# Performance work log

Hardware: AMD Instinct MI355X
Metric: run time of the kernel (lower is better)

## Reference

```python
import jax, jax.numpy as jnp
import numpy as np

B, C, W, H = 1024, 1, 128, 128
NUM_IDS = 64
MARGIN = 0.3


def setup_inputs() -> dict:
    key = jax.random.key(0)
    k1, k2 = jax.random.split(key)
    inputs = jax.random.normal(k1, (B, C, W, H), dtype=jnp.float32)
    targets = jax.random.randint(k2, (B,), 0, NUM_IDS, dtype=jnp.int32)
    return {"inputs": inputs, "targets": targets}


def _dc_align(anchor, other):
    # Batched cross-attention alignment (DCModuleOptimized assumption):
    # modi = softmax(anchor @ other^T / sqrt(h)) @ other, per sample.
    h = anchor.shape[-1]
    scale = 1.0 / jnp.sqrt(jnp.asarray(h, anchor.dtype))
    att = jax.nn.softmax(jnp.einsum('bij,bkj->bik', anchor, other) * scale, axis=-1)
    return jnp.einsum('bik,bkj->bij', att, other)


def reference(inputs, targets):
    b, c, w, h = inputs.shape
    x = inputs.reshape(b, -1)                      # (n, d); requires c == 1 downstream
    n = b
    # Pairwise Euclidean distances, stable clamp as in torch code
    sq = jnp.sum(x * x, axis=1)                    # (n,)
    dist = sq[:, None] + sq[None, :] - 2.0 * (x @ x.T)
    dist = jnp.sqrt(jnp.clip(dist, 1e-12, None))   # (n, n)
    mask = targets[:, None] == targets[None, :]    # (n, n) same-identity mask
    # Vectorized hard mining (replaces the per-row Python loop)
    NEG = jnp.asarray(-1e30, dist.dtype)
    POS = jnp.asarray(1e30, dist.dtype)
    hp_idx = jnp.argmax(jnp.where(mask, dist, NEG), axis=1)   # hardest positive per row
    hn_idx = jnp.argmin(jnp.where(mask, POS, dist), axis=1)   # hardest negative per row
    anchor = x.reshape(b, w, h)
    h_pos = anchor[hp_idx]                         # (b, w, h) gathered hard positives
    h_neg = anchor[hn_idx]                         # (b, w, h) gathered hard negatives
    # DC module applied over the whole batch at once
    modi_pos = _dc_align(anchor, h_pos)
    modi_neg = _dc_align(anchor, h_neg)
    dap = anchor.reshape(b, -1) - modi_pos.reshape(b, -1)
    dan = anchor.reshape(b, -1) - modi_neg.reshape(b, -1)
    dist_ap = jnp.sqrt(jnp.sum(dap * dap, axis=1))
    dist_an = jnp.sqrt(jnp.sum(dan * dan, axis=1))
    # MarginRankingLoss with y = 1: mean(relu(dist_ap - dist_an + margin))
    loss = jnp.mean(jax.nn.relu(dist_ap - dist_an + MARGIN))
    return loss
```

## Files before the change

### kernel.cpp

```cpp
#include <hip/hip_runtime.h>
#include <stdint.h>

#define NSAMP 1024
#define D 16384
#define WH 128
#define MARGIN 0.3f
#define KS 8
#define KSUB (D / KS)
#define SCALE 0.08838834764831845f
#define RSCALE 11.313708498984761f

typedef unsigned int uint;
typedef unsigned short ushort_t;

typedef __attribute__((ext_vector_type(8))) short bf16x8;
typedef __attribute__((ext_vector_type(4))) float f32x4;

__device__ __forceinline__ float bf2f(unsigned short b) {
    return __uint_as_float(((uint)b) << 16);
}
__device__ __forceinline__ unsigned short f2bf(float f) {
    uint u = __float_as_uint(f);
    u += 0x7fffu + ((u >> 16) & 1u);
    return (unsigned short)(u >> 16);
}
__device__ __forceinline__ void gload_lds16(const void* g, void* l) {
    __builtin_amdgcn_global_load_lds(
        (const __attribute__((address_space(1))) uint32_t*)g,
        (__attribute__((address_space(3))) uint32_t*)l, 16, 0, 0);
}
__device__ __forceinline__ bf16x8 bf8_half(bf16x8 v) {
    union { bf16x8 b; uint u[4]; } c;
    c.b = v;
    c.u[0] -= 0x00800080u; c.u[1] -= 0x00800080u;
    c.u[2] -= 0x00800080u; c.u[3] -= 0x00800080u;
    return c.b;
}
__device__ __forceinline__ int lds_off(int row, int col) {
    return row * 256 + ((((col >> 3) ^ (row & 15)) << 4) | ((col & 7) << 1));
}

__global__ __launch_bounds__(256) void k_norms_split(const float* __restrict__ x,
                                                     float* __restrict__ sq,
                                                     ushort_t* __restrict__ xhi,
                                                     ushort_t* __restrict__ xlo) {
    int b = blockIdx.x;
    int tid = threadIdx.x;
    const float* xr = x + (size_t)b * D;
    ushort_t* hr = xhi + (size_t)b * D;
    ushort_t* lr = xlo + (size_t)b * D;
    float s = 0.f;
    #pragma unroll
    for (int m = 0; m < 16; ++m) {
        int e = m * 1024 + tid * 4;
        float4 v = *(const float4*)(xr + e);
        s += v.x * v.x + v.y * v.y + v.z * v.z + v.w * v.w;
        ushort4 h, l;
        h.x = f2bf(v.x); l.x = f2bf(v.x - bf2f(h.x));
        h.y = f2bf(v.y); l.y = f2bf(v.y - bf2f(h.y));
        h.z = f2bf(v.z); l.z = f2bf(v.z - bf2f(h.z));
        h.w = f2bf(v.w); l.w = f2bf(v.w - bf2f(h.w));
        *(ushort4*)(hr + e) = h;
        *(ushort4*)(lr + e) = l;
    }
    for (int off = 32; off; off >>= 1) s += __shfl_down(s, off, 64);
    __shared__ float red[4];
    if ((tid & 63) == 0) red[tid >> 6] = s;
    __syncthreads();
    if (tid == 0) sq[b] = red[0] + red[1] + red[2] + red[3];
}

__global__ __launch_bounds__(256) void k_gram_mfma(const ushort_t* __restrict__ xhi,
                                                   const ushort_t* __restrict__ xlo,
                                                   float* __restrict__ Gp) {
    int lin = blockIdx.x + 8 * blockIdx.y + 64 * blockIdx.z;
    int ks = lin & 7, bi = (lin >> 3) & 7, bj = lin >> 6;
    int i0 = bi * 128, j0 = bj * 128;
    int tid = threadIdx.x;
    int w = tid >> 6, lane = tid & 63;
    int wm = w & 1, wn = w >> 1;
    int quad = lane >> 4, m16 = lane & 15;
    int srow = lane >> 2, sseg = lane & 3;

    __shared__ __align__(16) ushort_t Ahi_s[128 * 32];
    __shared__ __align__(16) ushort_t Bhi_s[128 * 32];
    __shared__ __align__(16) ushort_t Blo_s[128 * 32];

    f32x4 acc[4][4];
    #pragma unroll
    for (int ii = 0; ii < 4; ++ii)
        #pragma unroll
        for (int jj = 0; jj < 4; ++jj)
            acc[ii][jj] = (f32x4){0.f, 0.f, 0.f, 0.f};

    const size_t Abase = (size_t)i0 * D;
    const size_t Bbase = (size_t)j0 * D;

    for (int kb = 0; kb < KSUB / 32; ++kb) {
        int k0 = ks * KSUB + kb * 32;
        #pragma unroll
        for (int c = 0; c < 2; ++c) {
            int r = w * 32 + c * 16 + srow;
            size_t go = (size_t)r * D + k0 + sseg * 8;
            int lo = (w * 32 + c * 16) * 32;
            gload_lds16(xhi + Abase + go, &Ahi_s[lo]);
            gload_lds16(xhi + Bbase + go, &Bhi_s[lo]);
            gload_lds16(xlo + Bbase + go, &Blo_s[lo]);
        }
        __syncthreads();

        bf16x8 ah[4], bh[4], bl[4];
        #pragma unroll
        for (int ii = 0; ii < 4; ++ii) {
            int ar = wm * 64 + ii * 16 + m16;
            ah[ii] = *(const bf16x8*)&Ahi_s[ar * 32 + quad * 8];
        }
        #pragma unroll
        for (int jj = 0; jj < 4; ++jj) {
            int br = wn * 64 + jj * 16 + m16;
            bh[jj] = *(const bf16x8*)&Bhi_s[br * 32 + quad * 8];
            bl[jj] = *(const bf16x8*)&Blo_s[br * 32 + quad * 8];
        }
        #pragma unroll
        for (int ii = 0; ii < 4; ++ii) {
            bf16x8 ahh = bf8_half(ah[ii]);
            #pragma unroll
            for (int jj = 0; jj < 4; ++jj) {
                acc[ii][jj] = __builtin_amdgcn_mfma_f32_16x16x32_bf16(ahh, bh[jj], acc[ii][jj], 0, 0, 0);
                acc[ii][jj] = __builtin_amdgcn_mfma_f32_16x16x32_bf16(ah[ii], bl[jj], acc[ii][jj], 0, 0, 0);
            }
        }
        __syncthreads();
    }

    float* Gb = Gp + (size_t)ks * NSAMP * NSAMP;
    #pragma unroll
    for (int ii = 0; ii < 4; ++ii)
        #pragma unroll
        for (int jj = 0; jj < 4; ++jj) {
            int rg = i0 + wm * 64 + ii * 16 + quad * 4;
            int cg = j0 + wn * 64 + jj * 16 + m16;
            #pragma unroll
            for (int r = 0; r < 4; ++r)
                Gb[(size_t)(rg + r) * NSAMP + cg] = acc[ii][jj][r];
        }
}

__global__ __launch_bounds__(256) void k_fold_sym(const float* __restrict__ Gp,
                                                  float* __restrict__ G) {
    int J = blockIdx.x, I = blockIdx.y;
    int t = threadIdx.x;
    int r = t >> 4, c4 = (t & 15) * 4;
    __shared__ float TJ[64][65];
    float4 sIJ[4];
    #pragma unroll
    for (int rr = 0; rr < 4; ++rr) {
        int row = rr * 16 + r;
        size_t oIJ = (size_t)(I * 64 + row) * NSAMP + J * 64 + c4;
        size_t oJI = (size_t)(J * 64 + row) * NSAMP + I * 64 + c4;
        float4 a = {0.f, 0.f, 0.f, 0.f}, bb = {0.f, 0.f, 0.f, 0.f};
        #pragma unroll
        for (int p = 0; p < KS; ++p) {
            float4 v = *(const float4*)(Gp + (size_t)p * NSAMP * NSAMP + oIJ);
            float4 w = *(const float4*)(Gp + (size_t)p * NSAMP * NSAMP + oJI);
            a.x += v.x; a.y += v.y; a.z += v.z; a.w += v.w;
            bb.x += w.x; bb.y += w.y; bb.z += w.z; bb.w += w.w;
        }
        sIJ[rr] = a;
        TJ[row][c4 + 0] = bb.x; TJ[row][c4 + 1] = bb.y;
        TJ[row][c4 + 2] = bb.z; TJ[row][c4 + 3] = bb.w;
    }
    __syncthreads();
    #pragma unroll
    for (int rr = 0; rr < 4; ++rr) {
        int row = rr * 16 + r;
        float4 v = sIJ[rr];
        v.x += TJ[c4 + 0][row]; v.y += TJ[c4 + 1][row];
        v.z += TJ[c4 + 2][row]; v.w += TJ[c4 + 3][row];
        *(float4*)(G + (size_t)(I * 64 + row) * NSAMP + J * 64 + c4) = v;
    }
}

__global__ void k_select(const float* __restrict__ G,
                         const float* __restrict__ sq, const int* __restrict__ tgt,
                         int* __restrict__ hp, int* __restrict__ hn,
                         float* __restrict__ dsq) {
    int i = blockIdx.x;
    int tid = threadIdx.x;
    float sqi = sq[i];
    int ti = tgt[i];
    float pv = -3.0e38f; int pj = 0x7FFFFFFF;
    float nv = 3.0e38f;  int nj = 0x7FFFFFFF;
    #pragma unroll
    for (int m = 0; m < 4; ++m) {
        int j = tid + 256 * m;
        float g = G[(size_t)i * NSAMP + j];
        float d2 = sqi + sq[j] - 2.f * g;
        float d = sqrtf(fmaxf(d2, 1e-12f));
        bool same = (tgt[j] == ti);
        float cp = same ? d : -1e30f;
        float cn = same ? 1e30f : d;
        if (cp > pv || (cp == pv && j < pj)) { pv = cp; pj = j; }
        if (cn < nv || (cn == nv && j < nj)) { nv = cn; nj = j; }
    }
    for (int off = 32; off; off >>= 1) {
        float opv = __shfl_down(pv, off, 64); int opj = __shfl_down(pj, off, 64);
        float onv = __shfl_down(nv, off, 64); int onj = __shfl_down(nj, off, 64);
        if (opv > pv || (opv == pv && opj < pj)) { pv = opv; pj = opj; }
        if (onv < nv || (onv == nv && onj < nj)) { nv = onv; nj = onj; }
    }
    __shared__ float spv[4], snv[4];
    __shared__ int spj[4], snj[4];
    if ((tid & 63) == 0) { int wv = tid >> 6; spv[wv] = pv; spj[wv] = pj; snv[wv] = nv; snj[wv] = nj; }
    __syncthreads();
    if (tid == 0) {
        for (int wv = 1; wv < 4; ++wv) {
            if (spv[wv] > pv || (spv[wv] == pv && spj[wv] < pj)) { pv = spv[wv]; pj = spj[wv]; }
            if (snv[wv] < nv || (snv[wv] == nv && snj[wv] < nj)) { nv = snv[wv]; nj = snj[wv]; }
        }
        hp[i] = pj; hn[i] = nj;
        dsq[i] = sqi; dsq[NSAMP + i] = sqi;
    }
}

__global__ __launch_bounds__(256) void k_dc_mfma(const ushort_t* __restrict__ xhi,
                                                 const int* __restrict__ hp,
                                                 const int* __restrict__ hn,
                                                 float* __restrict__ dsq) {
    int b = blockIdx.x;
    int which = blockIdx.y;
    int oidx = (which == 0) ? hp[b] : hn[b];
    const ushort_t* Ag = xhi + (size_t)b * D;
    const ushort_t* Og = xhi + (size_t)oidx * D;

    __shared__ __align__(16) char smem[32768];

    int tid = threadIdx.x;
    int wv = tid >> 6, lane = tid & 63;
    int quad = lane >> 4, m16 = lane & 15;

    bf16x8 af[2][4];
    #pragma unroll
    for (int tj2 = 0; tj2 < 2; ++tj2) {
        int r = (2 * wv + tj2) * 16 + m16;
        #pragma unroll
        for (int ks = 0; ks < 4; ++ks)
            af[tj2][ks] = *(const bf16x8*)(Ag + r * WH + ks * 32 + quad * 8);
    }

    uint4 stg[8];
    #pragma unroll
    for (int k = 0; k < 8; ++k)
        stg[k] = *(const uint4*)((const char*)Og + (size_t)(tid + 256 * k) * 16);
    #pragma unroll
    for (int k = 0; k < 8; ++k) {
        int g = tid + 256 * k;
        *(uint4*)(smem + lds_off(g >> 4, (g & 15) * 8)) = stg[k];
    }
    __syncthreads();

    f32x4 accS[8][2];
    #pragma unroll
    for (int ti = 0; ti < 8; ++ti)
        #pragma unroll
        for (int tj2 = 0; tj2 < 2; ++tj2)
            accS[ti][tj2] = (f32x4){0.f, 0.f, 0.f, 0.f};
    #pragma unroll
    for (int ks = 0; ks < 4; ++ks) {
        bf16x8 of[8];
        #pragma unroll
        for (int ti = 0; ti < 8; ++ti)
            of[ti] = *(const bf16x8*)(smem + lds_off(ti * 16 + m16, (ks * 4 + quad) * 8));
        #pragma unroll
        for (int ti = 0; ti < 8; ++ti)
            #pragma unroll
            for (int tj2 = 0; tj2 < 2; ++tj2)
                accS[ti][tj2] = __builtin_amdgcn_mfma_f32_16x16x32_bf16(of[ti], af[tj2][ks], accS[ti][tj2], 0, 0, 0);
    }

    int c0 = (tid & 31) * 4, h0 = (tid >> 5) * 16;
    uint4 trd[4][2];
    #pragma unroll
    for (int j = 0; j < 4; ++j)
        #pragma unroll
        for (int k = 0; k < 2; ++k)
            trd[j][k] = *(const uint4*)(smem + lds_off(c0 + j, h0 + 8 * k));
    __syncthreads();

    #pragma unroll
    for (int i = 0; i < 16; ++i) {
        uint v[4];
        #pragma unroll
        for (int j = 0; j < 4; ++j) {
            uint wo = ((const uint*)&trd[j][i >> 3])[(i >> 1) & 3];
            v[j] = (i & 1) ? (wo >> 16) : (wo & 0xffffu);
        }
        uint2 pk;
        pk.x = v[0] | (v[1] << 16);
        pk.y = v[2] | (v[3] << 16);
        *(uint2*)(smem + lds_off(h0 + i, c0)) = pk;
    }

    float tpart = 0.f;
    bf16x8 pf[2][4];
    #pragma unroll
    for (int tj2 = 0; tj2 < 2; ++tj2) {
        float mx = -3.0e38f;
        #pragma unroll
        for (int ti = 0; ti < 8; ++ti)
            #pragma unroll
            for (int r = 0; r < 4; ++r) {
                float s = accS[ti][tj2][r] * SCALE;
                accS[ti][tj2][r] = s;
                mx = fmaxf(mx, s);
            }
        mx = fmaxf(mx, __shfl_xor(mx, 16, 64));
        mx = fmaxf(mx, __shfl_xor(mx, 32, 64));
        float sum = 0.f, tnum = 0.f;
        #pragma unroll
        for (int ti = 0; ti < 8; ++ti)
            #pragma unroll
            for (int r = 0; r < 4; ++r) {
                float s = accS[ti][tj2][r];
                float e = __expf(s - mx);
                accS[ti][tj2][r] = e;
                sum += e;
                tnum += s * e;
            }
        sum += __shfl_xor(sum, 16, 64);
        sum += __shfl_xor(sum, 32, 64);
        tnum += __shfl_xor(tnum, 16, 64);
        tnum += __shfl_xor(tnum, 32, 64);
        float inv = 1.f / sum;
        tpart += 0.25f * tnum * inv;

        uint Ep[8][2];
        #pragma unroll
        for (int ti = 0; ti < 8; ++ti) {
            Ep[ti][0] = (uint)f2bf(accS[ti][tj2][0] * inv) |
                        ((uint)f2bf(accS[ti][tj2][1] * inv) << 16);
            Ep[ti][1] = (uint)f2bf(accS[ti][tj2][2] * inv) |
                        ((uint)f2bf(accS[ti][tj2][3] * inv) << 16);
        }
        int tih = quad >> 1;
        #pragma unroll
        for (int ks = 0; ks < 4; ++ks) {
            union { uint u[4]; bf16x8 v; } fr;
            #pragma unroll
            for (int k = 0; k < 4; ++k) {
                int src = (((quad << 1) + (k >> 1)) & 3) * 16 + m16;
                int a = __shfl((int)Ep[2 * ks + 0][k & 1], src, 64);
                int bsh = __shfl((int)Ep[2 * ks + 1][k & 1], src, 64);
                fr.u[k] = (uint)((tih == 0) ? a : bsh);
            }
            pf[tj2][ks] = fr.v;
        }
    }
    __syncthreads();

    f32x4 accM[2][8];
    #pragma unroll
    for (int tj2 = 0; tj2 < 2; ++tj2)
        #pragma unroll
        for (int tj = 0; tj < 8; ++tj)
            accM[tj2][tj] = (f32x4){0.f, 0.f, 0.f, 0.f};
    #pragma unroll
    for (int ks = 0; ks < 4; ++ks) {
        bf16x8 otf[8];
        #pragma unroll
        for (int tj = 0; tj < 8; ++tj)
            otf[tj] = *(const bf16x8*)(smem + lds_off(tj * 16 + m16, (ks * 4 + quad) * 8));
        #pragma unroll
        for (int tj2 = 0; tj2 < 2; ++tj2)
            #pragma unroll
            for (int tj = 0; tj < 8; ++tj)
                accM[tj2][tj] = __builtin_amdgcn_mfma_f32_16x16x32_bf16(pf[tj2][ks], otf[tj], accM[tj2][tj], 0, 0, 0);
    }

    float m2 = 0.f;
    #pragma unroll
    for (int tj2 = 0; tj2 < 2; ++tj2)
        #pragma unroll
        for (int tj = 0; tj < 8; ++tj)
            #pragma unroll
            for (int r = 0; r < 4; ++r) {
                float mvv = accM[tj2][tj][r];
                m2 += mvv * mvv;
            }
    float part = m2 - 2.f * RSCALE * tpart;
    for (int off = 32; off; off >>= 1) part += __shfl_down(part, off, 64);
    if (lane == 0) atomicAdd(&dsq[which * NSAMP + b], part);
}

__global__ void k_loss(const float* __restrict__ dsq, float* __restrict__ out) {
    int tid = threadIdx.x;
    float s = 0.f;
    #pragma unroll
    for (int m = 0; m < 4; ++m) {
        int b = tid + 256 * m;
        float ap = sqrtf(fmaxf(dsq[b], 0.f));
        float an = sqrtf(fmaxf(dsq[NSAMP + b], 0.f));
        s += fmaxf(ap - an + MARGIN, 0.f);
    }
    for (int off = 32; off; off >>= 1) s += __shfl_down(s, off, 64);
    __shared__ float red[4];
    if ((tid & 63) == 0) red[tid >> 6] = s;
    __syncthreads();
    if (tid == 0) out[0] = (red[0] + red[1] + red[2] + red[3]) * (1.f / NSAMP);
}

extern "C" void kernel_launch(void* const* d_in, const int* in_sizes, int n_in,
                              void* d_out, int out_size, void* d_ws, size_t ws_size,
                              hipStream_t stream) {
    const float* x = (const float*)d_in[0];
    const int* tgt = (const int*)d_in[1];
    float* out = (float*)d_out;
    char* ws = (char*)d_ws;

    float* Gp = (float*)ws;
    ushort_t* xhi = (ushort_t*)(ws + (size_t)32 * 1024 * 1024);
    ushort_t* xlo = xhi + (size_t)NSAMP * D;
    float* G = (float*)xlo;
    float* sq = (float*)(ws + (size_t)96 * 1024 * 1024);
    float* dsq = sq + NSAMP;
    int* hp = (int*)(dsq + 2 * NSAMP);
    int* hn = hp + NSAMP;

    k_norms_split<<<NSAMP, 256, 0, stream>>>(x, sq, xhi, xlo);
    k_gram_mfma<<<dim3(8, 8, 8), 256, 0, stream>>>(xhi, xlo, Gp);
    k_fold_sym<<<dim3(16, 16), 256, 0, stream>>>(Gp, G);
    k_select<<<NSAMP, 256, 0, stream>>>(G, sq, tgt, hp, hn, dsq);
    k_dc_mfma<<<dim3(NSAMP, 2), 256, 0, stream>>>(xhi, hp, hn, dsq);
    k_loss<<<1, 256, 0, stream>>>(dsq, out);
}
```

Before: 233.3 us.

## Compute only lower-triangular Gram tiles with adaptive split-K and fuse DC passes

The Gram kernel now computes only the 36 lower-triangular 128x128 tiles instead of all 64. Diagonal tiles use a symmetric hi/lo trick, and off-diagonal tiles use three MFMA products. Split-K depth rises to 16 when the workspace allows, and the fold kernel reconstructs the full symmetric matrix from compact per-tile partials. The DC kernel now handles the positive and negative pairs in one block, which replaces the atomics and the dsq initialisation in k_select. The cost is more MFMAs per off-diagonal tile and a second pass through LDS per block.

```diff
diff --git a/kernel.cpp b/kernel.cpp
--- a/kernel.cpp
+++ b/kernel.cpp
@@ -5,8 +5,7 @@
 #define D 16384
 #define WH 128
 #define MARGIN 0.3f
-#define KS 8
-#define KSUB (D / KS)
+#define NTILES 36
 #define SCALE 0.08838834764831845f
 #define RSCALE 11.313708498984761f
 
@@ -70,11 +69,17 @@
     if (tid == 0) sq[b] = red[0] + red[1] + red[2] + red[3];
 }
 
-__global__ __launch_bounds__(256) void k_gram_mfma(const ushort_t* __restrict__ xhi,
-                                                   const ushort_t* __restrict__ xlo,
-                                                   float* __restrict__ Gp) {
-    int lin = blockIdx.x + 8 * blockIdx.y + 64 * blockIdx.z;
-    int ks = lin & 7, bi = (lin >> 3) & 7, bj = lin >> 6;
+__global__ __launch_bounds__(256) void k_gram_tri(const ushort_t* __restrict__ xhi,
+                                                  const ushort_t* __restrict__ xlo,
+                                                  float* __restrict__ Gp,
+                                                  int ksmask, int ksshift, int ksub) {
+    int lin = blockIdx.x;
+    int ks = lin & ksmask;
+    int t = lin >> ksshift;
+    int bi = 0;
+    while (t >= ((bi + 1) * (bi + 2)) / 2) ++bi;
+    int bj = t - (bi * (bi + 1)) / 2;
+    bool diag = (bi == bj);
     int i0 = bi * 128, j0 = bj * 128;
     int tid = threadIdx.x;
     int w = tid >> 6, lane = tid & 63;
@@ -83,6 +88,7 @@
     int srow = lane >> 2, sseg = lane & 3;
 
     __shared__ __align__(16) ushort_t Ahi_s[128 * 32];
+    __shared__ __align__(16) ushort_t Alo_s[128 * 32];
     __shared__ __align__(16) ushort_t Bhi_s[128 * 32];
     __shared__ __align__(16) ushort_t Blo_s[128 * 32];
 
@@ -96,16 +102,19 @@
     const size_t Abase = (size_t)i0 * D;
     const size_t Bbase = (size_t)j0 * D;
 
-    for (int kb = 0; kb < KSUB / 32; ++kb) {
-        int k0 = ks * KSUB + kb * 32;
+    for (int kb = 0; kb < ksub / 32; ++kb) {
+        int k0 = ks * ksub + kb * 32;
         #pragma unroll
         for (int c = 0; c < 2; ++c) {
             int r = w * 32 + c * 16 + srow;
             size_t go = (size_t)r * D + k0 + sseg * 8;
             int lo = (w * 32 + c * 16) * 32;
             gload_lds16(xhi + Abase + go, &Ahi_s[lo]);
-            gload_lds16(xhi + Bbase + go, &Bhi_s[lo]);
             gload_lds16(xlo + Bbase + go, &Blo_s[lo]);
+            if (!diag) {
+                gload_lds16(xhi + Bbase + go, &Bhi_s[lo]);
+                gload_lds16(xlo + Abase + go, &Alo_s[lo]);
+            }
         }
         __syncthreads();
 
@@ -115,40 +124,65 @@
             int ar = wm * 64 + ii * 16 + m16;
             ah[ii] = *(const bf16x8*)&Ahi_s[ar * 32 + quad * 8];
         }
+        const ushort_t* Bh = diag ? Ahi_s : Bhi_s;
         #pragma unroll
         for (int jj = 0; jj < 4; ++jj) {
             int br = wn * 64 + jj * 16 + m16;
-            bh[jj] = *(const bf16x8*)&Bhi_s[br * 32 + quad * 8];
+            bh[jj] = *(const bf16x8*)&Bh[br * 32 + quad * 8];
             bl[jj] = *(const bf16x8*)&Blo_s[br * 32 + quad * 8];
         }
-        #pragma unroll
-        for (int ii = 0; ii < 4; ++ii) {
-            bf16x8 ahh = bf8_half(ah[ii]);
-            #pragma unroll
-            for (int jj = 0; jj < 4; ++jj) {
-                acc[ii][jj] = __builtin_amdgcn_mfma_f32_16x16x32_bf16(ahh, bh[jj], acc[ii][jj], 0, 0, 0);
-                acc[ii][jj] = __builtin_amdgcn_mfma_f32_16x16x32_bf16(ah[ii], bl[jj], acc[ii][jj], 0, 0, 0);
-            }
+        if (diag) {
+            #pragma unroll
+            for (int ii = 0; ii < 4; ++ii) {
+                bf16x8 ahh = bf8_half(ah[ii]);
+                #pragma unroll
+                for (int jj = 0; jj < 4; ++jj) {
+                    acc[ii][jj] = __builtin_amdgcn_mfma_f32_16x16x32_bf16(ahh, bh[jj], acc[ii][jj], 0, 0, 0);
+                    acc[ii][jj] = __builtin_amdgcn_mfma_f32_16x16x32_bf16(ah[ii], bl[jj], acc[ii][jj], 0, 0, 0);
+                }
+            }
+        } else {
+            bf16x8 al[4];
+            #pragma unroll
+            for (int ii = 0; ii < 4; ++ii) {
+                int ar = wm * 64 + ii * 16 + m16;
+                al[ii] = *(const bf16x8*)&Alo_s[ar * 32 + quad * 8];
+            }
+            #pragma unroll
+            for (int ii = 0; ii < 4; ++ii)
+                #pragma unroll
+                for (int jj = 0; jj < 4; ++jj) {
+                    acc[ii][jj] = __builtin_amdgcn_mfma_f32_16x16x32_bf16(ah[ii], bh[jj], acc[ii][jj], 0, 0, 0);
+                    acc[ii][jj] = __builtin_amdgcn_mfma_f32_16x16x32_bf16(ah[ii], bl[jj], acc[ii][jj], 0, 0, 0);
+                    acc[ii][jj] = __builtin_amdgcn_mfma_f32_16x16x32_bf16(al[ii], bh[jj], acc[ii][jj], 0, 0, 0);
+                }
         }
         __syncthreads();
     }
 
-    float* Gb = Gp + (size_t)ks * NSAMP * NSAMP;
+    float* Gb = Gp + ((size_t)ks * NTILES + t) * 16384;
     #pragma unroll
     for (int ii = 0; ii < 4; ++ii)
         #pragma unroll
         for (int jj = 0; jj < 4; ++jj) {
-            int rg = i0 + wm * 64 + ii * 16 + quad * 4;
-            int cg = j0 + wn * 64 + jj * 16 + m16;
+            int rg = wm * 64 + ii * 16 + quad * 4;
+            int cg = wn * 64 + jj * 16 + m16;
             #pragma unroll
             for (int r = 0; r < 4; ++r)
-                Gb[(size_t)(rg + r) * NSAMP + cg] = acc[ii][jj][r];
-        }
-}
-
-__global__ __launch_bounds__(256) void k_fold_sym(const float* __restrict__ Gp,
-                                                  float* __restrict__ G) {
+                Gb[(size_t)(rg + r) * 128 + cg] = acc[ii][jj][r];
+        }
+}
+
+__global__ __launch_bounds__(256) void k_fold_tri(const float* __restrict__ Gp,
+                                                  float* __restrict__ G, int nks) {
     int J = blockIdx.x, I = blockIdx.y;
+    int bi = I >> 1, bj = J >> 1;
+    int li = I & 1, lj = J & 1;
+    bool wantD = (bi >= bj);
+    bool wantT = (bi <= bj);
+    int tD = wantD ? (bi * (bi + 1)) / 2 + bj : 0;
+    int tT = wantT ? (bj * (bj + 1)) / 2 + bi : 0;
+
     int t = threadIdx.x;
     int r = t >> 4, c4 = (t & 15) * 4;
     __shared__ float TJ[64][65];
@@ -156,15 +190,22 @@
     #pragma unroll
     for (int rr = 0; rr < 4; ++rr) {
         int row = rr * 16 + r;
-        size_t oIJ = (size_t)(I * 64 + row) * NSAMP + J * 64 + c4;
-        size_t oJI = (size_t)(J * 64 + row) * NSAMP + I * 64 + c4;
         float4 a = {0.f, 0.f, 0.f, 0.f}, bb = {0.f, 0.f, 0.f, 0.f};
-        #pragma unroll
-        for (int p = 0; p < KS; ++p) {
-            float4 v = *(const float4*)(Gp + (size_t)p * NSAMP * NSAMP + oIJ);
-            float4 w = *(const float4*)(Gp + (size_t)p * NSAMP * NSAMP + oJI);
-            a.x += v.x; a.y += v.y; a.z += v.z; a.w += v.w;
-            bb.x += w.x; bb.y += w.y; bb.z += w.z; bb.w += w.w;
+        if (wantD) {
+            size_t off = (size_t)(li * 64 + row) * 128 + lj * 64 + c4;
+            #pragma unroll 4
+            for (int p = 0; p < nks; ++p) {
+                float4 v = *(const float4*)(Gp + ((size_t)p * NTILES + tD) * 16384 + off);
+                a.x += v.x; a.y += v.y; a.z += v.z; a.w += v.w;
+            }
+        }
+        if (wantT) {
+            size_t off = (size_t)(lj * 64 + row) * 128 + li * 64 + c4;
+            #pragma unroll 4
+            for (int p = 0; p < nks; ++p) {
+                float4 v = *(const float4*)(Gp + ((size_t)p * NTILES + tT) * 16384 + off);
+                bb.x += v.x; bb.y += v.y; bb.z += v.z; bb.w += v.w;
+            }
         }
         sIJ[rr] = a;
         TJ[row][c4 + 0] = bb.x; TJ[row][c4 + 1] = bb.y;
@@ -175,16 +216,17 @@
     for (int rr = 0; rr < 4; ++rr) {
         int row = rr * 16 + r;
         float4 v = sIJ[rr];
-        v.x += TJ[c4 + 0][row]; v.y += TJ[c4 + 1][row];
-        v.z += TJ[c4 + 2][row]; v.w += TJ[c4 + 3][row];
+        if (wantT) {
+            v.x += TJ[c4 + 0][row]; v.y += TJ[c4 + 1][row];
+            v.z += TJ[c4 + 2][row]; v.w += TJ[c4 + 3][row];
+        }
         *(float4*)(G + (size_t)(I * 64 + row) * NSAMP + J * 64 + c4) = v;
     }
 }
 
 __global__ void k_select(const float* __restrict__ G,
                          const float* __restrict__ sq, const int* __restrict__ tgt,
-                         int* __restrict__ hp, int* __restrict__ hn,
-                         float* __restrict__ dsq) {
+                         int* __restrict__ hp, int* __restrict__ hn) {
     int i = blockIdx.x;
     int tid = threadIdx.x;
     float sqi = sq[i];
@@ -219,21 +261,19 @@
             if (snv[wv] < nv || (snv[wv] == nv && snj[wv] < nj)) { nv = snv[wv]; nj = snj[wv]; }
         }
         hp[i] = pj; hn[i] = nj;
-        dsq[i] = sqi; dsq[NSAMP + i] = sqi;
     }
 }
 
 __global__ __launch_bounds__(256) void k_dc_mfma(const ushort_t* __restrict__ xhi,
                                                  const int* __restrict__ hp,
                                                  const int* __restrict__ hn,
+                                                 const float* __restrict__ sq,
                                                  float* __restrict__ dsq) {
     int b = blockIdx.x;
-    int which = blockIdx.y;
-    int oidx = (which == 0) ? hp[b] : hn[b];
     const ushort_t* Ag = xhi + (size_t)b * D;
-    const ushort_t* Og = xhi + (size_t)oidx * D;
 
     __shared__ __align__(16) char smem[32768];
+    __shared__ float red2[2][4];
 
     int tid = threadIdx.x;
     int wv = tid >> 6, lane = tid & 63;
@@ -248,148 +288,159 @@
             af[tj2][ks] = *(const bf16x8*)(Ag + r * WH + ks * 32 + quad * 8);
     }
 
-    uint4 stg[8];
-    #pragma unroll
-    for (int k = 0; k < 8; ++k)
-        stg[k] = *(const uint4*)((const char*)Og + (size_t)(tid + 256 * k) * 16);
-    #pragma unroll
-    for (int k = 0; k < 8; ++k) {
-        int g = tid + 256 * k;
-        *(uint4*)(smem + lds_off(g >> 4, (g & 15) * 8)) = stg[k];
+    for (int which = 0; which < 2; ++which) {
+        int oidx = (which == 0) ? hp[b] : hn[b];
+        const ushort_t* Og = xhi + (size_t)oidx * D;
+
+        uint4 stg[8];
+        #pragma unroll
+        for (int k = 0; k < 8; ++k)
+            stg[k] = *(const uint4*)((const char*)Og + (size_t)(tid + 256 * k) * 16);
+        if (which) __syncthreads();
+        #pragma unroll
+        for (int k = 0; k < 8; ++k) {
+            int g = tid + 256 * k;
+            *(uint4*)(smem + lds_off(g >> 4, (g & 15) * 8)) = stg[k];
+        }
+        __syncthreads();
+
+        f32x4 accS[8][2];
+        #pragma unroll
+        for (int ti = 0; ti < 8; ++ti)
+            #pragma unroll
+            for (int tj2 = 0; tj2 < 2; ++tj2)
+                accS[ti][tj2] = (f32x4){0.f, 0.f, 0.f, 0.f};
+        #pragma unroll
+        for (int ks = 0; ks < 4; ++ks) {
+            bf16x8 of[8];
+            #pragma unroll
+            for (int ti = 0; ti < 8; ++ti)
+                of[ti] = *(const bf16x8*)(smem + lds_off(ti * 16 + m16, (ks * 4 + quad) * 8));
+            #pragma unroll
+            for (int ti = 0; ti < 8; ++ti)
+                #pragma unroll
+                for (int tj2 = 0; tj2 < 2; ++tj2)
+                    accS[ti][tj2] = __builtin_amdgcn_mfma_f32_16x16x32_bf16(of[ti], af[tj2][ks], accS[ti][tj2], 0, 0, 0);
+        }
+
+        int c0 = (tid & 31) * 4, h0 = (tid >> 5) * 16;
+        uint4 trd[4][2];
+        #pragma unroll
+        for (int j = 0; j < 4; ++j)
+            #pragma unroll
+            for (int k = 0; k < 2; ++k)
+                trd[j][k] = *(const uint4*)(smem + lds_off(c0 + j, h0 + 8 * k));
+        __syncthreads();
+
+        #pragma unroll
+        for (int i = 0; i < 16; ++i) {
+            uint v[4];
+            #pragma unroll
+            for (int j = 0; j < 4; ++j) {
+                uint wo = ((const uint*)&trd[j][i >> 3])[(i >> 1) & 3];
+                v[j] = (i & 1) ? (wo >> 16) : (wo & 0xffffu);
+            }
+            uint2 pk;
+            pk.x = v[0] | (v[1] << 16);
+            pk.y = v[2] | (v[3] << 16);
+            *(uint2*)(smem + lds_off(h0 + i, c0)) = pk;
+        }
+
+        float tpart = 0.f;
+        bf16x8 pf[2][4];
+        #pragma unroll
+        for (int tj2 = 0; tj2 < 2; ++tj2) {
+            float mx = -3.0e38f;
+            #pragma unroll
+            for (int ti = 0; ti < 8; ++ti)
+                #pragma unroll
+                for (int r = 0; r < 4; ++r) {
+                    float s = accS[ti][tj2][r] * SCALE;
+                    accS[ti][tj2][r] = s;
+                    mx = fmaxf(mx, s);
+                }
+            mx = fmaxf(mx, __shfl_xor(mx, 16, 64));
+            mx = fmaxf(mx, __shfl_xor(mx, 32, 64));
+            float sum = 0.f, tnum = 0.f;
+            #pragma unroll
+            for (int ti = 0; ti < 8; ++ti)
+                #pragma unroll
+                for (int r = 0; r < 4; ++r) {
+                    float s = accS[ti][tj2][r];
+                    float e = __expf(s - mx);
+                    accS[ti][tj2][r] = e;
+                    sum += e;
+                    tnum += s * e;
+                }
+            sum += __shfl_xor(sum, 16, 64);
+            sum += __shfl_xor(sum, 32, 64);
+            tnum += __shfl_xor(tnum, 16, 64);
+            tnum += __shfl_xor(tnum, 32, 64);
+            float inv = 1.f / sum;
+            tpart += 0.25f * tnum * inv;
+
+            uint Ep[8][2];
+            #pragma unroll
+            for (int ti = 0; ti < 8; ++ti) {
+                Ep[ti][0] = (uint)f2bf(accS[ti][tj2][0] * inv) |
+                            ((uint)f2bf(accS[ti][tj2][1] * inv) << 16);
+                Ep[ti][1] = (uint)f2bf(accS[ti][tj2][2] * inv) |
+                            ((uint)f2bf(accS[ti][tj2][3] * inv) << 16);
+            }
+            int tih = quad >> 1;
+            #pragma unroll
+            for (int ks = 0; ks < 4; ++ks) {
+                union { uint u[4]; bf16x8 v; } fr;
+                #pragma unroll
+                for (int k = 0; k < 4; ++k) {
+                    int src = (((quad << 1) + (k >> 1)) & 3) * 16 + m16;
+                    int a = __shfl((int)Ep[2 * ks + 0][k & 1], src, 64);
+                    int bsh = __shfl((int)Ep[2 * ks + 1][k & 1], src, 64);
+                    fr.u[k] = (uint)((tih == 0) ? a : bsh);
+                }
+                pf[tj2][ks] = fr.v;
+            }
+        }
+        __syncthreads();
+
+        f32x4 accM[2][8];
+        #pragma unroll
+        for (int tj2 = 0; tj2 < 2; ++tj2)
+            #pragma unroll
+            for (int tj = 0; tj < 8; ++tj)
+                accM[tj2][tj] = (f32x4){0.f, 0.f, 0.f, 0.f};
+        #pragma unroll
+        for (int ks = 0; ks < 4; ++ks) {
+            bf16x8 otf[8];
+            #pragma unroll
+            for (int tj = 0; tj < 8; ++tj)
+                otf[tj] = *(const bf16x8*)(smem + lds_off(tj * 16 + m16, (ks * 4 + quad) * 8));
+            #pragma unroll
+            for (int tj2 = 0; tj2 < 2; ++tj2)
+                #pragma unroll
+                for (int tj = 0; tj < 8; ++tj)
+                    accM[tj2][tj] = __builtin_amdgcn_mfma_f32_16x16x32_bf16(pf[tj2][ks], otf[tj], accM[tj2][tj], 0, 0, 0);
+        }
+
+        float m2 = 0.f;
+        #pragma unroll
+        for (int tj2 = 0; tj2 < 2; ++tj2)
+            #pragma unroll
+            for (int tj = 0; tj < 8; ++tj)
+                #pragma unroll
+                for (int r = 0; r < 4; ++r) {
+                    float mvv = accM[tj2][tj][r];
+                    m2 += mvv * mvv;
+                }
+        float part = m2 - 2.f * RSCALE * tpart;
+        for (int off = 32; off; off >>= 1) part += __shfl_down(part, off, 64);
+        if (lane == 0) red2[which][wv] = part;
     }
     __syncthreads();
-
-    f32x4 accS[8][2];
-    #pragma unroll
-    for (int ti = 0; ti < 8; ++ti)
-        #pragma unroll
-        for (int tj2 = 0; tj2 < 2; ++tj2)
-            accS[ti][tj2] = (f32x4){0.f, 0.f, 0.f, 0.f};
-    #pragma unroll
-    for (int ks = 0; ks < 4; ++ks) {
-        bf16x8 of[8];
-        #pragma unroll
-        for (int ti = 0; ti < 8; ++ti)
-            of[ti] = *(const bf16x8*)(smem + lds_off(ti * 16 + m16, (ks * 4 + quad) * 8));
-        #pragma unroll
-        for (int ti = 0; ti < 8; ++ti)
-            #pragma unroll
-            for (int tj2 = 0; tj2 < 2; ++tj2)
-                accS[ti][tj2] = __builtin_amdgcn_mfma_f32_16x16x32_bf16(of[ti], af[tj2][ks], accS[ti][tj2], 0, 0, 0);
-    }
-
-    int c0 = (tid & 31) * 4, h0 = (tid >> 5) * 16;
-    uint4 trd[4][2];
-    #pragma unroll
-    for (int j = 0; j < 4; ++j)
-        #pragma unroll
-        for (int k = 0; k < 2; ++k)
-            trd[j][k] = *(const uint4*)(smem + lds_off(c0 + j, h0 + 8 * k));
-    __syncthreads();
-
-    #pragma unroll
-    for (int i = 0; i < 16; ++i) {
-        uint v[4];
-        #pragma unroll
-        for (int j = 0; j < 4; ++j) {
-            uint wo = ((const uint*)&trd[j][i >> 3])[(i >> 1) & 3];
-            v[j] = (i & 1) ? (wo >> 16) : (wo & 0xffffu);
-        }
-        uint2 pk;
-        pk.x = v[0] | (v[1] << 16);
-        pk.y = v[2] | (v[3] << 16);
-        *(uint2*)(smem + lds_off(h0 + i, c0)) = pk;
-    }
-
-    float tpart = 0.f;
-    bf16x8 pf[2][4];
-    #pragma unroll
-    for (int tj2 = 0; tj2 < 2; ++tj2) {
-        float mx = -3.0e38f;
-        #pragma unroll
-        for (int ti = 0; ti < 8; ++ti)
-            #pragma unroll
-            for (int r = 0; r < 4; ++r) {
-                float s = accS[ti][tj2][r] * SCALE;
-                accS[ti][tj2][r] = s;
-                mx = fmaxf(mx, s);
-            }
-        mx = fmaxf(mx, __shfl_xor(mx, 16, 64));
-        mx = fmaxf(mx, __shfl_xor(mx, 32, 64));
-        float sum = 0.f, tnum = 0.f;
-        #pragma unroll
-        for (int ti = 0; ti < 8; ++ti)
-            #pragma unroll
-            for (int r = 0; r < 4; ++r) {
-                float s = accS[ti][tj2][r];
-                float e = __expf(s - mx);
-                accS[ti][tj2][r] = e;
-                sum += e;
-                tnum += s * e;
-            }
-        sum += __shfl_xor(sum, 16, 64);
-        sum += __shfl_xor(sum, 32, 64);
-        tnum += __shfl_xor(tnum, 16, 64);
-        tnum += __shfl_xor(tnum, 32, 64);
-        float inv = 1.f / sum;
-        tpart += 0.25f * tnum * inv;
-
-        uint Ep[8][2];
-        #pragma unroll
-        for (int ti = 0; ti < 8; ++ti) {
-            Ep[ti][0] = (uint)f2bf(accS[ti][tj2][0] * inv) |
-                        ((uint)f2bf(accS[ti][tj2][1] * inv) << 16);
-            Ep[ti][1] = (uint)f2bf(accS[ti][tj2][2] * inv) |
-                        ((uint)f2bf(accS[ti][tj2][3] * inv) << 16);
-        }
-        int tih = quad >> 1;
-        #pragma unroll
-        for (int ks = 0; ks < 4; ++ks) {
-            union { uint u[4]; bf16x8 v; } fr;
-            #pragma unroll
-            for (int k = 0; k < 4; ++k) {
-                int src = (((quad << 1) + (k >> 1)) & 3) * 16 + m16;
-                int a = __shfl((int)Ep[2 * ks + 0][k & 1], src, 64);
-                int bsh = __shfl((int)Ep[2 * ks + 1][k & 1], src, 64);
-                fr.u[k] = (uint)((tih == 0) ? a : bsh);
-            }
-            pf[tj2][ks] = fr.v;
-        }
-    }
-    __syncthreads();
-
-    f32x4 accM[2][8];
-    #pragma unroll
-    for (int tj2 = 0; tj2 < 2; ++tj2)
-        #pragma unroll
-        for (int tj = 0; tj < 8; ++tj)
-            accM[tj2][tj] = (f32x4){0.f, 0.f, 0.f, 0.f};
-    #pragma unroll
-    for (int ks = 0; ks < 4; ++ks) {
-        bf16x8 otf[8];
-        #pragma unroll
-        for (int tj = 0; tj < 8; ++tj)
-            otf[tj] = *(const bf16x8*)(smem + lds_off(tj * 16 + m16, (ks * 4 + quad) * 8));
-        #pragma unroll
-        for (int tj2 = 0; tj2 < 2; ++tj2)
-            #pragma unroll
-            for (int tj = 0; tj < 8; ++tj)
-                accM[tj2][tj] = __builtin_amdgcn_mfma_f32_16x16x32_bf16(pf[tj2][ks], otf[tj], accM[tj2][tj], 0, 0, 0);
-    }
-
-    float m2 = 0.f;
-    #pragma unroll
-    for (int tj2 = 0; tj2 < 2; ++tj2)
-        #pragma unroll
-        for (int tj = 0; tj < 8; ++tj)
-            #pragma unroll
-            for (int r = 0; r < 4; ++r) {
-                float mvv = accM[tj2][tj][r];
-                m2 += mvv * mvv;
-            }
-    float part = m2 - 2.f * RSCALE * tpart;
-    for (int off = 32; off; off >>= 1) part += __shfl_down(part, off, 64);
-    if (lane == 0) atomicAdd(&dsq[which * NSAMP + b], part);
+    if (tid < 2) {
+        float p = red2[tid][0] + red2[tid][1] + red2[tid][2] + red2[tid][3];
+        dsq[tid * NSAMP + b] = sq[b] + p;
+    }
 }
 
 __global__ void k_loss(const float* __restrict__ dsq, float* __restrict__ out) {
@@ -417,19 +468,26 @@
     float* out = (float*)d_out;
     char* ws = (char*)d_ws;
 
+    const size_t XB = (size_t)NSAMP * D * 2;
+    size_t gp16 = (size_t)16 * NTILES * 16384 * 4;
+    size_t gp8 = (size_t)8 * NTILES * 16384 * 4;
+    int nks = (ws_size >= gp16 + 2 * XB + (size_t)65536) ? 16 : 8;
+    size_t gpb = (nks == 16) ? gp16 : gp8;
+
     float* Gp = (float*)ws;
-    ushort_t* xhi = (ushort_t*)(ws + (size_t)32 * 1024 * 1024);
-    ushort_t* xlo = xhi + (size_t)NSAMP * D;
+    ushort_t* xhi = (ushort_t*)(ws + gpb);
+    ushort_t* xlo = (ushort_t*)(ws + gpb + XB);
     float* G = (float*)xlo;
-    float* sq = (float*)(ws + (size_t)96 * 1024 * 1024);
+    float* sq = (float*)(ws + gpb + 2 * XB);
     float* dsq = sq + NSAMP;
     int* hp = (int*)(dsq + 2 * NSAMP);
     int* hn = hp + NSAMP;
 
     k_norms_split<<<NSAMP, 256, 0, stream>>>(x, sq, xhi, xlo);
-    k_gram_mfma<<<dim3(8, 8, 8), 256, 0, stream>>>(xhi, xlo, Gp);
-    k_fold_sym<<<dim3(16, 16), 256, 0, stream>>>(Gp, G);
-    k_select<<<NSAMP, 256, 0, stream>>>(G, sq, tgt, hp, hn, dsq);
-    k_dc_mfma<<<dim3(NSAMP, 2), 256, 0, stream>>>(xhi, hp, hn, dsq);
+    k_gram_tri<<<NTILES * nks, 256, 0, stream>>>(xhi, xlo, Gp, nks - 1,
+                                                 (nks == 16) ? 4 : 3, D / nks);
+    k_fold_tri<<<dim3(16, 16), 256, 0, stream>>>(Gp, G, nks);
+    k_select<<<NSAMP, 256, 0, stream>>>(G, sq, tgt, hp, hn);
+    k_dc_mfma<<<NSAMP, 256, 0, stream>>>(xhi, hp, hn, sq, dsq);
     k_loss<<<1, 256, 0, stream>>>(dsq, out);
 }
```

Result: slower. 288.5 us (+23.7%).
